# Performance work log

Hardware: AMD Instinct MI355X
Metric: run time of the kernel (lower is better)

## Reference

```python
import jax, jax.numpy as jnp
import numpy as np

H = 16
D_MODEL = 1024
HEAD_DIM = D_MODEL // H
NEG = -1e9


def setup_inputs() -> dict:
    key = jax.random.key(0)
    k1, k2, k3, k4, k5, k6 = jax.random.split(key, 6)
    B, L = 2, 2048
    feature = jax.random.normal(k1, (B, L, D_MODEL), dtype=jnp.float32)
    mask = jax.random.randint(k2, (B, L), 0, 2, dtype=jnp.int32)
    # Linear weights stored torch-style as [out, in]; biases zero-init per initialize().
    s = 1.0 / np.sqrt(D_MODEL)
    W_Q = jax.random.uniform(k3, (D_MODEL, D_MODEL), jnp.float32, -s, s)
    W_K = jax.random.uniform(k4, (D_MODEL, D_MODEL), jnp.float32, -s, s)
    W_V = jax.random.uniform(k5, (D_MODEL, D_MODEL), jnp.float32, -s, s)
    b_Q = jnp.zeros((D_MODEL,), jnp.float32)
    b_K = jnp.zeros((D_MODEL,), jnp.float32)
    b_V = jnp.zeros((D_MODEL,), jnp.float32)
    return {"feature": feature, "mask": mask, "W_Q": W_Q, "b_Q": b_Q,
            "W_K": W_K, "b_K": b_K, "W_V": W_V, "b_V": b_V}


def reference(feature, mask, W_Q, b_Q, W_K, b_K, W_V, b_V):
    B, L, _ = feature.shape
    scale = jnp.sqrt(jnp.float32(HEAD_DIM))
    # Projections: torch Linear is x @ W^T + b. Split into heads: [B, H, L, Dh]
    def proj(W, b):
        y = feature @ W.T + b
        return y.reshape(B, L, H, HEAD_DIM).transpose(0, 2, 1, 3)
    Q = proj(W_Q, b_Q)
    K = proj(W_K, b_K)
    V = proj(W_V, b_V)
    # Scores [B, H, Lq, Lk]
    A = jnp.einsum('bhqd,bhkd->bhqk', Q, K) / scale
    # Key-side mask broadcast over heads and query positions
    A = jnp.where(mask[:, None, None, :] == 0, jnp.float32(NEG), A)
    alpha = jax.nn.softmax(A, axis=-1)
    out = jnp.einsum('bhqk,bhkd->bhqd', alpha, V)  # [B, H, L, Dh]
    return out.transpose(0, 2, 1, 3).reshape(B, L, H * HEAD_DIM)
```

## Files before the change

kernel.cpp:

```cpp
#include <hip/hip_runtime.h>

typedef __bf16 bf16;
typedef __attribute__((ext_vector_type(4))) __bf16 bf16x4;
typedef __attribute__((ext_vector_type(8))) __bf16 bf16x8;
typedef __attribute__((ext_vector_type(4))) float f32x4;
typedef __attribute__((ext_vector_type(16))) float f32x16;
typedef unsigned int u32;

#define D_MODEL 1024
#define SEQ_L   2048
#define NHEAD   16
#define HDIM    64
#define MROWS   4096

#define S_SCALE 0.18033688f

#define FEAT_OFF  512u
#define WQ_OFF    (FEAT_OFF + 4194304u)
#define WK_OFF    (WQ_OFF + 1048576u)
#define WV_OFF    (WK_OFF + 1048576u)
#define BQ_OFF    (WV_OFF + 1048576u)
#define BK_OFF    (BQ_OFF + 1024u)
#define BV_OFF    (BK_OFF + 1024u)
#define Q_OFF     (BV_OFF + 1024u)
#define K_OFF     (Q_OFF + 4194304u)
#define V_OFF     (K_OFF + 4194304u)

typedef const __attribute__((address_space(1))) u32* gp_t;
typedef __attribute__((address_space(3))) u32* lp_t;
__device__ __forceinline__ void ld16(const bf16* g, bf16* l) {
    __builtin_amdgcn_global_load_lds((gp_t)g, (lp_t)l, 16, 0, 0);
}

__global__ void convert_in(const float* __restrict__ feat,
                           const float* __restrict__ wq, const float* __restrict__ wk,
                           const float* __restrict__ wv,
                           const float* __restrict__ bq, const float* __restrict__ bk,
                           const float* __restrict__ bv,
                           bf16* __restrict__ ws) {
    const int bid = blockIdx.x;
    const float* src; bf16* dst; int off; float sc = 1.0f;
    if (bid < 4096)      { src = feat; dst = ws + FEAT_OFF; off = bid * 1024; }
    else if (bid < 5120) { src = wq;   dst = ws + WQ_OFF;   off = (bid - 4096) * 1024; sc = S_SCALE; }
    else if (bid < 6144) { src = wk;   dst = ws + WK_OFF;   off = (bid - 5120) * 1024; }
    else if (bid < 7168) { src = wv;   dst = ws + WV_OFF;   off = (bid - 6144) * 1024; }
    else if (bid == 7168){ src = bq;   dst = ws + BQ_OFF;   off = 0; sc = S_SCALE; }
    else if (bid == 7169){ src = bk;   dst = ws + BK_OFF;   off = 0; }
    else                 { src = bv;   dst = ws + BV_OFF;   off = 0; }
    int idx = off + threadIdx.x * 4;
    float4 v = *(const float4*)(src + idx);
    dst[idx + 0] = (bf16)(v.x * sc);
    dst[idx + 1] = (bf16)(v.y * sc);
    dst[idx + 2] = (bf16)(v.z * sc);
    dst[idx + 3] = (bf16)(v.w * sc);
}

__global__ __launch_bounds__(256, 2) void qkv_gemm(const bf16* __restrict__ ws,
                                                   bf16* __restrict__ wsw,
                                                   const int* __restrict__ mask) {
    const int zi = blockIdx.z;
    const bf16* Amat = (zi == 2) ? ws + WV_OFF : ws + FEAT_OFF;
    const bf16* Bmat = (zi == 0) ? ws + WQ_OFF : (zi == 1) ? ws + WK_OFF : ws + FEAT_OFF;
    const bf16* bias = ws + ((zi == 0) ? BQ_OFF : (zi == 1) ? BK_OFF : BV_OFF);
    bf16* Y = (zi == 2) ? wsw + V_OFF : wsw + Q_OFF + (size_t)zi * 4194304u;

    __shared__ bf16 Alds[128 * 64];
    __shared__ bf16 Blds[128 * 64];

    const int t    = threadIdx.x;
    const int lane = t & 63;
    const int wave = t >> 6;
    const int quad = lane >> 4;
    const int l16  = lane & 15;
    const int m0   = ((zi == 2) ? blockIdx.y : blockIdx.x) * 128;
    const int n0   = ((zi == 2) ? blockIdx.x : blockIdx.y) * 128;
    const int wrow = (wave >> 1) * 64;
    const int wcol = (wave & 1) * 64;

    const int r8 = lane >> 3;
    const int sl = lane & 7;
    const int sg = sl ^ r8;

    f32x4 acc[4][4];
    for (int mi = 0; mi < 4; ++mi)
        for (int ni = 0; ni < 4; ++ni)
            acc[mi][ni] = (f32x4){0.f, 0.f, 0.f, 0.f};

    for (int k0 = 0; k0 < D_MODEL; k0 += 64) {
#pragma unroll
        for (int i = 0; i < 4; ++i) {
            int ch  = wave * 4 + i;
            int row = ch * 8 + r8;
            ld16(Amat + (size_t)(m0 + row) * D_MODEL + k0 + sg * 8, Alds + ch * 512);
            ld16(Bmat + (size_t)(n0 + row) * D_MODEL + k0 + sg * 8, Blds + ch * 512);
        }
        __syncthreads();

#pragma unroll
        for (int kk = 0; kk < 2; ++kk) {
            const int sgb = quad + kk * 4;
            bf16x8 af[4], bfr[4];
#pragma unroll
            for (int mi = 0; mi < 4; ++mi) {
                int row = wrow + mi * 16 + l16;
                af[mi] = *(const bf16x8*)(&Alds[row * 64 + ((sgb ^ (row & 7)) << 3)]);
            }
#pragma unroll
            for (int ni = 0; ni < 4; ++ni) {
                int row = wcol + ni * 16 + l16;
                bfr[ni] = *(const bf16x8*)(&Blds[row * 64 + ((sgb ^ (row & 7)) << 3)]);
            }
#pragma unroll
            for (int mi = 0; mi < 4; ++mi)
#pragma unroll
                for (int ni = 0; ni < 4; ++ni)
                    acc[mi][ni] = __builtin_amdgcn_mfma_f32_16x16x32_bf16(
                        af[mi], bfr[ni], acc[mi][ni], 0, 0, 0);
        }
        __syncthreads();
    }

    if (zi < 2) {
#pragma unroll
        for (int ni = 0; ni < 4; ++ni) {
            int col = n0 + wcol + ni * 16 + l16;
            float bvf = (float)bias[col];
#pragma unroll
            for (int mi = 0; mi < 4; ++mi) {
                int rowb = m0 + wrow + mi * 16 + quad * 4;
#pragma unroll
                for (int r = 0; r < 4; ++r) {
                    float v = acc[mi][ni][r] + bvf;
                    if (zi == 1 && mask[rowb + r] == 0) v = 0.f;
                    Y[(size_t)(rowb + r) * D_MODEL + col] = (bf16)v;
                }
            }
        }
    } else {
#pragma unroll
        for (int mi = 0; mi < 4; ++mi) {
#pragma unroll
            for (int r = 0; r < 4; ++r) {
                int rowv = m0 + wrow + mi * 16 + quad * 4 + r;
                float bvf = (float)bias[rowv];
#pragma unroll
                for (int ni = 0; ni < 4; ++ni) {
                    int col = n0 + wcol + ni * 16 + l16;
                    float v = acc[mi][ni][r] + bvf;
                    if (mask[col] == 0) v = 0.f;
                    size_t addr = (size_t)(col >> 11) * 2097152u +
                                  (size_t)rowv * 2048u + (col & 2047);
                    Y[addr] = (bf16)v;
                }
            }
        }
    }
}

__global__ __launch_bounds__(256, 4) void attn_kernel(
    const bf16* __restrict__ ws, bf16* __restrict__ wsw,
    const int* __restrict__ mask, float* __restrict__ out) {
    const int bh  = blockIdx.x;
    const int qt  = blockIdx.y;
    const int ks2 = blockIdx.z;
    const int b   = bh >> 4, h = bh & 15;
    const int t    = threadIdx.x;
    const int lane = t & 63;
    const int wave = t >> 6;
    const int half = lane >> 5;
    const int l31  = lane & 31;
    const int kt0  = ks2 * 1024;

    __shared__ bf16 Klds[2][64 * 64];
    __shared__ bf16 Vlds[2][64 * 64];

    const bf16* Qh  = ws + Q_OFF + (size_t)(b * SEQ_L) * D_MODEL + h * HDIM;
    const bf16* Kh  = ws + K_OFF + (size_t)(b * SEQ_L) * D_MODEL + h * HDIM;
    const bf16* Vth = ws + V_OFF + (size_t)b * 2097152u + (size_t)(h * HDIM) * SEQ_L;

    const int qrow0 = qt * 128 + wave * 32;
    bf16x8 qf[4];
#pragma unroll
    for (int ks = 0; ks < 4; ++ks)
        qf[ks] = *(const bf16x8*)(Qh + (size_t)(qrow0 + l31) * D_MODEL
                                  + ks * 16 + half * 8);

    bf16x8 ones;
#pragma unroll
    for (int j = 0; j < 8; ++j) ones[j] = (bf16)1.0f;

    f32x16 o[2], lacc;
    int nm = 0;
#pragma unroll
    for (int i = 0; i < 16; ++i) { o[0][i] = 0.f; o[1][i] = 0.f; lacc[i] = 0.f; }

    const int srow = (lane >> 3);
    const int sg   = (lane & 7) ^ srow;

#define STAGE(bb, kt)                                                          \
    do {                                                                       \
        _Pragma("unroll")                                                      \
        for (int i = 0; i < 2; ++i) {                                          \
            int row = i * 32 + wave * 8 + srow;                                \
            ld16(Kh + (size_t)((kt) + row) * D_MODEL + sg * 8,                 \
                 &Klds[bb][i * 2048 + wave * 512]);                            \
            ld16(Vth + (size_t)row * SEQ_L + (kt) + sg * 8,                    \
                 &Vlds[bb][i * 2048 + wave * 512]);                            \
        }                                                                      \
    } while (0)

    STAGE(0, kt0);
    __syncthreads();

    int cur = 0;
    for (int kt = kt0; kt < kt0 + 1024; kt += 64) {
        if (kt + 64 < kt0 + 1024) STAGE(cur ^ 1, kt + 64);

        int mv = mask[b * SEQ_L + kt + lane];
        nm += (int)__popcll(__ballot(mv != 0));

        f32x16 st[2];
#pragma unroll
        for (int ktile = 0; ktile < 2; ++ktile) {
#pragma unroll
            for (int i = 0; i < 16; ++i) st[ktile][i] = 0.f;
#pragma unroll
            for (int ks = 0; ks < 4; ++ks) {
                const int row  = ktile * 32 + l31;
                const int slot = (ks * 2 + half) ^ (l31 & 7);
                bf16x8 kf = *(const bf16x8*)(&Klds[cur][row * 64 + slot * 8]);
                st[ktile] = __builtin_amdgcn_mfma_f32_32x32x16_bf16(
                    kf, qf[ks], st[ktile], 0, 0, 0);
            }
        }

        bf16x4 pk[2][4];
#pragma unroll
        for (int ktile = 0; ktile < 2; ++ktile) {
#pragma unroll
            for (int g = 0; g < 4; ++g) {
                bf16x4 pkv;
#pragma unroll
                for (int j = 0; j < 4; ++j)
                    pkv[j] = (bf16)__builtin_amdgcn_exp2f(st[ktile][g * 4 + j]);
                pk[ktile][g] = pkv;
            }
        }

        bf16x8 pf[4];
#pragma unroll
        for (int ks = 0; ks < 4; ++ks) {
            const int k1 = ks & 1, kt2 = ks >> 1;
            uint2 a  = __builtin_bit_cast(uint2, pk[kt2][2 * k1]);
            uint2 bb = __builtin_bit_cast(uint2, pk[kt2][2 * k1 + 1]);
            uint2 keep, send;
            keep.x = half ? bb.x : a.x;  keep.y = half ? bb.y : a.y;
            send.x = half ? a.x : bb.x;  send.y = half ? a.y : bb.y;
            uint2 recv;
            recv.x = (unsigned)__shfl_xor((int)send.x, 32);
            recv.y = (unsigned)__shfl_xor((int)send.y, 32);
            uint4 frag;
            frag.x = half ? recv.x : keep.x;
            frag.y = half ? recv.y : keep.y;
            frag.z = half ? keep.x : recv.x;
            frag.w = half ? keep.y : recv.y;
            pf[ks] = __builtin_bit_cast(bf16x8, frag);
        }

#pragma unroll
        for (int ks = 0; ks < 4; ++ks)
            lacc = __builtin_amdgcn_mfma_f32_32x32x16_bf16(pf[ks], ones, lacc, 0, 0, 0);
#pragma unroll
        for (int dt = 0; dt < 2; ++dt) {
#pragma unroll
            for (int ks = 0; ks < 4; ++ks) {
                const int row  = dt * 32 + l31;
                const int slot = (ks * 2 + half) ^ (l31 & 7);
                bf16x8 vf = *(const bf16x8*)(&Vlds[cur][row * 64 + slot * 8]);
                o[dt] = __builtin_amdgcn_mfma_f32_32x32x16_bf16(
                    pf[ks], vf, o[dt], 0, 0, 0);
            }
        }

        __syncthreads();
        cur ^= 1;
    }
#undef STAGE

    float* Lp  = (float*)(wsw + WQ_OFF);
    bf16*  O1  = wsw + FEAT_OFF;
    const float corr = (float)(1024 - nm);
#pragma unroll
    for (int r = 0; r < 16; ++r) {
        const int q32 = (r & 3) + 8 * (r >> 2) + 4 * half;
        const int q = qrow0 + q32;
        const size_t base = ((size_t)(b * SEQ_L + q)) * D_MODEL + h * HDIM;
        if (l31 == 0)
            Lp[ks2 * 65536 + bh * 2048 + qrow0 + q32] = lacc[r] - corr;
        if (ks2 == 0) {
            out[base + l31]      = o[0][r];
            out[base + 32 + l31] = o[1][r];
        } else {
            O1[base + l31]      = (bf16)o[0][r];
            O1[base + 32 + l31] = (bf16)o[1][r];
        }
    }
}

__global__ void combine(float* __restrict__ out, const bf16* __restrict__ ws) {
    const float* Lp = (const float*)(ws + WQ_OFF);
    const bf16*  O1 = ws + FEAT_OFF;
    int idx = (blockIdx.x * 256 + threadIdx.x) * 4;
    int row = idx >> 10;
    int col = idx & 1023;
    int b = row >> 11, q = row & 2047, h = col >> 6;
    int li = (b * 16 + h) * 2048 + q;
    float rl = 1.0f / fmaxf(Lp[li] + Lp[65536 + li], 1e-30f);
    float4 o0 = *(float4*)(out + idx);
    bf16x4 o1 = *(const bf16x4*)(O1 + idx);
    float4 res;
    res.x = (o0.x + (float)o1[0]) * rl;
    res.y = (o0.y + (float)o1[1]) * rl;
    res.z = (o0.z + (float)o1[2]) * rl;
    res.w = (o0.w + (float)o1[3]) * rl;
    *(float4*)(out + idx) = res;
}

extern "C" void kernel_launch(void* const* d_in, const int* in_sizes, int n_in,
                              void* d_out, int out_size, void* d_ws, size_t ws_size,
                              hipStream_t stream) {
    const float* feat = (const float*)d_in[0];
    const int*   mask = (const int*)d_in[1];
    const float* Wq = (const float*)d_in[2];
    const float* bq = (const float*)d_in[3];
    const float* Wk = (const float*)d_in[4];
    const float* bk = (const float*)d_in[5];
    const float* Wv = (const float*)d_in[6];
    const float* bv = (const float*)d_in[7];

    bf16* ws = (bf16*)d_ws;

    convert_in<<<7171, 256, 0, stream>>>(feat, Wq, Wk, Wv, bq, bk, bv, ws);

    dim3 g1(32, 8, 3);
    qkv_gemm<<<g1, 256, 0, stream>>>(ws, ws, mask);

    dim3 g2(2 * NHEAD, SEQ_L / 128, 2);
    attn_kernel<<<g2, 256, 0, stream>>>(ws, ws, mask, (float*)d_out);

    combine<<<4096, 256, 0, stream>>>((float*)d_out, ws);
}
```

Before: 173.6 us.

## Process two query tiles per wave in attention, sum softmax row on VALU

Each wave now handles 64 query rows (two 32-row tiles), so every K/V fragment read from LDS feeds two MFMAs, and the grid shrinks to half as many blocks. The row-sum of exp values is accumulated with VALU adds and reduced with a cross-half shuffle instead of an extra MFMA against a ones vector. Key-tile iteration starts at a per-block rotated phase to spread memory traffic, s_setprio brackets the MFMA sections, and the convert kernel now writes bf16x4 vector stores. The cost is higher register pressure (launch bounds lowered to 2 blocks per SM) and fewer blocks for occupancy.

```diff
diff --git a/kernel.cpp b/kernel.cpp
--- a/kernel.cpp
+++ b/kernel.cpp
@@ -49,10 +49,12 @@
     else                 { src = bv;   dst = ws + BV_OFF;   off = 0; }
     int idx = off + threadIdx.x * 4;
     float4 v = *(const float4*)(src + idx);
-    dst[idx + 0] = (bf16)(v.x * sc);
-    dst[idx + 1] = (bf16)(v.y * sc);
-    dst[idx + 2] = (bf16)(v.z * sc);
-    dst[idx + 3] = (bf16)(v.w * sc);
+    bf16x4 o;
+    o[0] = (bf16)(v.x * sc);
+    o[1] = (bf16)(v.y * sc);
+    o[2] = (bf16)(v.z * sc);
+    o[3] = (bf16)(v.w * sc);
+    *(bf16x4*)(dst + idx) = o;
 }
 
 __global__ __launch_bounds__(256, 2) void qkv_gemm(const bf16* __restrict__ ws,
@@ -157,7 +159,43 @@
     }
 }
 
-__global__ __launch_bounds__(256, 4) void attn_kernel(
+__device__ __forceinline__ void softmax_pack(const f32x16* st, f32x4& ls,
+                                             bf16x8* pf, const int half) {
+    bf16x4 pk[2][4];
+#pragma unroll
+    for (int ktile = 0; ktile < 2; ++ktile)
+#pragma unroll
+        for (int g = 0; g < 4; ++g) {
+            bf16x4 pkv;
+#pragma unroll
+            for (int j = 0; j < 4; ++j) {
+                float e = __builtin_amdgcn_exp2f(st[ktile][g * 4 + j]);
+                ls[j] += e;
+                pkv[j] = (bf16)e;
+            }
+            pk[ktile][g] = pkv;
+        }
+#pragma unroll
+    for (int ks = 0; ks < 4; ++ks) {
+        const int k1 = ks & 1, kt2 = ks >> 1;
+        uint2 a  = __builtin_bit_cast(uint2, pk[kt2][2 * k1]);
+        uint2 bb = __builtin_bit_cast(uint2, pk[kt2][2 * k1 + 1]);
+        uint2 keep, send;
+        keep.x = half ? bb.x : a.x;  keep.y = half ? bb.y : a.y;
+        send.x = half ? a.x : bb.x;  send.y = half ? a.y : bb.y;
+        uint2 recv;
+        recv.x = (unsigned)__shfl_xor((int)send.x, 32);
+        recv.y = (unsigned)__shfl_xor((int)send.y, 32);
+        uint4 frag;
+        frag.x = half ? recv.x : keep.x;
+        frag.y = half ? recv.y : keep.y;
+        frag.z = half ? keep.x : recv.x;
+        frag.w = half ? keep.y : recv.y;
+        pf[ks] = __builtin_bit_cast(bf16x8, frag);
+    }
+}
+
+__global__ __launch_bounds__(256, 2) void attn_kernel(
     const bf16* __restrict__ ws, bf16* __restrict__ wsw,
     const int* __restrict__ mask, float* __restrict__ out) {
     const int bh  = blockIdx.x;
@@ -178,21 +216,24 @@
     const bf16* Kh  = ws + K_OFF + (size_t)(b * SEQ_L) * D_MODEL + h * HDIM;
     const bf16* Vth = ws + V_OFF + (size_t)b * 2097152u + (size_t)(h * HDIM) * SEQ_L;
 
-    const int qrow0 = qt * 128 + wave * 32;
-    bf16x8 qf[4];
-#pragma unroll
-    for (int ks = 0; ks < 4; ++ks)
-        qf[ks] = *(const bf16x8*)(Qh + (size_t)(qrow0 + l31) * D_MODEL
-                                  + ks * 16 + half * 8);
-
-    bf16x8 ones;
-#pragma unroll
-    for (int j = 0; j < 8; ++j) ones[j] = (bf16)1.0f;
-
-    f32x16 o[2], lacc;
+    const int qrowA = qt * 256 + wave * 64;
+    const int qrowB = qrowA + 32;
+    bf16x8 qfA[4], qfB[4];
+#pragma unroll
+    for (int ks = 0; ks < 4; ++ks) {
+        qfA[ks] = *(const bf16x8*)(Qh + (size_t)(qrowA + l31) * D_MODEL
+                                   + ks * 16 + half * 8);
+        qfB[ks] = *(const bf16x8*)(Qh + (size_t)(qrowB + l31) * D_MODEL
+                                   + ks * 16 + half * 8);
+    }
+
+    f32x16 oA[2], oB[2];
+    f32x4  lsA = (f32x4){0.f, 0.f, 0.f, 0.f};
+    f32x4  lsB = (f32x4){0.f, 0.f, 0.f, 0.f};
     int nm = 0;
 #pragma unroll
-    for (int i = 0; i < 16; ++i) { o[0][i] = 0.f; o[1][i] = 0.f; lacc[i] = 0.f; }
+    for (int i = 0; i < 16; ++i) { oA[0][i] = 0.f; oA[1][i] = 0.f;
+                                   oB[0][i] = 0.f; oB[1][i] = 0.f; }
 
     const int srow = (lane >> 3);
     const int sg   = (lane & 7) ^ srow;
@@ -209,67 +250,48 @@
         }                                                                      \
     } while (0)
 
-    STAGE(0, kt0);
+    const int phase = (bh * 5 + qt * 3 + ks2 * 9) & 15;
+
+    STAGE(0, kt0 + (phase << 6));
     __syncthreads();
 
     int cur = 0;
-    for (int kt = kt0; kt < kt0 + 1024; kt += 64) {
-        if (kt + 64 < kt0 + 1024) STAGE(cur ^ 1, kt + 64);
+    for (int it = 0; it < 16; ++it) {
+        const int kt = kt0 + (((it + phase) & 15) << 6);
+        if (it < 15) {
+            const int ktn = kt0 + (((it + 1 + phase) & 15) << 6);
+            STAGE(cur ^ 1, ktn);
+        }
 
         int mv = mask[b * SEQ_L + kt + lane];
         nm += (int)__popcll(__ballot(mv != 0));
 
-        f32x16 st[2];
+        f32x16 stA[2], stB[2];
+#pragma unroll
+        for (int ktile = 0; ktile < 2; ++ktile)
+#pragma unroll
+            for (int i = 0; i < 16; ++i) { stA[ktile][i] = 0.f; stB[ktile][i] = 0.f; }
+        __builtin_amdgcn_s_setprio(1);
 #pragma unroll
         for (int ktile = 0; ktile < 2; ++ktile) {
-#pragma unroll
-            for (int i = 0; i < 16; ++i) st[ktile][i] = 0.f;
 #pragma unroll
             for (int ks = 0; ks < 4; ++ks) {
                 const int row  = ktile * 32 + l31;
                 const int slot = (ks * 2 + half) ^ (l31 & 7);
                 bf16x8 kf = *(const bf16x8*)(&Klds[cur][row * 64 + slot * 8]);
-                st[ktile] = __builtin_amdgcn_mfma_f32_32x32x16_bf16(
-                    kf, qf[ks], st[ktile], 0, 0, 0);
-            }
-        }
-
-        bf16x4 pk[2][4];
-#pragma unroll
-        for (int ktile = 0; ktile < 2; ++ktile) {
-#pragma unroll
-            for (int g = 0; g < 4; ++g) {
-                bf16x4 pkv;
-#pragma unroll
-                for (int j = 0; j < 4; ++j)
-                    pkv[j] = (bf16)__builtin_amdgcn_exp2f(st[ktile][g * 4 + j]);
-                pk[ktile][g] = pkv;
-            }
-        }
-
-        bf16x8 pf[4];
-#pragma unroll
-        for (int ks = 0; ks < 4; ++ks) {
-            const int k1 = ks & 1, kt2 = ks >> 1;
-            uint2 a  = __builtin_bit_cast(uint2, pk[kt2][2 * k1]);
-            uint2 bb = __builtin_bit_cast(uint2, pk[kt2][2 * k1 + 1]);
-            uint2 keep, send;
-            keep.x = half ? bb.x : a.x;  keep.y = half ? bb.y : a.y;
-            send.x = half ? a.x : bb.x;  send.y = half ? a.y : bb.y;
-            uint2 recv;
-            recv.x = (unsigned)__shfl_xor((int)send.x, 32);
-            recv.y = (unsigned)__shfl_xor((int)send.y, 32);
-            uint4 frag;
-            frag.x = half ? recv.x : keep.x;
-            frag.y = half ? recv.y : keep.y;
-            frag.z = half ? keep.x : recv.x;
-            frag.w = half ? keep.y : recv.y;
-            pf[ks] = __builtin_bit_cast(bf16x8, frag);
-        }
-
-#pragma unroll
-        for (int ks = 0; ks < 4; ++ks)
-            lacc = __builtin_amdgcn_mfma_f32_32x32x16_bf16(pf[ks], ones, lacc, 0, 0, 0);
+                stA[ktile] = __builtin_amdgcn_mfma_f32_32x32x16_bf16(
+                    kf, qfA[ks], stA[ktile], 0, 0, 0);
+                stB[ktile] = __builtin_amdgcn_mfma_f32_32x32x16_bf16(
+                    kf, qfB[ks], stB[ktile], 0, 0, 0);
+            }
+        }
+        __builtin_amdgcn_s_setprio(0);
+
+        bf16x8 pfA[4], pfB[4];
+        softmax_pack(stA, lsA, pfA, half);
+        softmax_pack(stB, lsB, pfB, half);
+
+        __builtin_amdgcn_s_setprio(1);
 #pragma unroll
         for (int dt = 0; dt < 2; ++dt) {
 #pragma unroll
@@ -277,10 +299,13 @@
                 const int row  = dt * 32 + l31;
                 const int slot = (ks * 2 + half) ^ (l31 & 7);
                 bf16x8 vf = *(const bf16x8*)(&Vlds[cur][row * 64 + slot * 8]);
-                o[dt] = __builtin_amdgcn_mfma_f32_32x32x16_bf16(
-                    pf[ks], vf, o[dt], 0, 0, 0);
-            }
-        }
+                oA[dt] = __builtin_amdgcn_mfma_f32_32x32x16_bf16(
+                    pfA[ks], vf, oA[dt], 0, 0, 0);
+                oB[dt] = __builtin_amdgcn_mfma_f32_32x32x16_bf16(
+                    pfB[ks], vf, oB[dt], 0, 0, 0);
+            }
+        }
+        __builtin_amdgcn_s_setprio(0);
 
         __syncthreads();
         cur ^= 1;
@@ -290,19 +315,38 @@
     float* Lp  = (float*)(wsw + WQ_OFF);
     bf16*  O1  = wsw + FEAT_OFF;
     const float corr = (float)(1024 - nm);
+    float lA = lsA[0] + lsA[1] + lsA[2] + lsA[3];
+    float lB = lsB[0] + lsB[1] + lsB[2] + lsB[3];
+    lA += __shfl_xor(lA, 32);
+    lB += __shfl_xor(lB, 32);
+    if (half == 0) {
+        Lp[ks2 * 65536 + bh * 2048 + qrowA + l31] = lA - corr;
+        Lp[ks2 * 65536 + bh * 2048 + qrowB + l31] = lB - corr;
+    }
 #pragma unroll
     for (int r = 0; r < 16; ++r) {
         const int q32 = (r & 3) + 8 * (r >> 2) + 4 * half;
-        const int q = qrow0 + q32;
-        const size_t base = ((size_t)(b * SEQ_L + q)) * D_MODEL + h * HDIM;
-        if (l31 == 0)
-            Lp[ks2 * 65536 + bh * 2048 + qrow0 + q32] = lacc[r] - corr;
-        if (ks2 == 0) {
-            out[base + l31]      = o[0][r];
-            out[base + 32 + l31] = o[1][r];
-        } else {
-            O1[base + l31]      = (bf16)o[0][r];
-            O1[base + 32 + l31] = (bf16)o[1][r];
+        {
+            const int q = qrowA + q32;
+            const size_t base = ((size_t)(b * SEQ_L + q)) * D_MODEL + h * HDIM;
+            if (ks2 == 0) {
+                out[base + l31]      = oA[0][r];
+                out[base + 32 + l31] = oA[1][r];
+            } else {
+                O1[base + l31]      = (bf16)oA[0][r];
+                O1[base + 32 + l31] = (bf16)oA[1][r];
+            }
+        }
+        {
+            const int q = qrowB + q32;
+            const size_t base = ((size_t)(b * SEQ_L + q)) * D_MODEL + h * HDIM;
+            if (ks2 == 0) {
+                out[base + l31]      = oB[0][r];
+                out[base + 32 + l31] = oB[1][r];
+            } else {
+                O1[base + l31]      = (bf16)oB[0][r];
+                O1[base + 32 + l31] = (bf16)oB[1][r];
+            }
         }
     }
 }
@@ -345,7 +389,7 @@
     dim3 g1(32, 8, 3);
     qkv_gemm<<<g1, 256, 0, stream>>>(ws, ws, mask);
 
-    dim3 g2(2 * NHEAD, SEQ_L / 128, 2);
+    dim3 g2(2 * NHEAD, SEQ_L / 256, 2);
     attn_kernel<<<g2, 256, 0, stream>>>(ws, ws, mask, (float*)d_out);
 
     combine<<<4096, 256, 0, stream>>>((float*)d_out, ws);
```

Result: no change. 172.7 us (-0.5%).

## Software-pipeline QK^T one tile ahead with triple-buffered K in attention

Applied to the files above, without the earlier changes.

The attention loop is restructured so the QK^T MFMAs for the next key tile are issued before the PV MFMAs of the current tile. This lets the exp/pack work overlap with matrix-core work. K is now triple-buffered and staged two tiles ahead, V stays double-buffered, and the loop is fully unrolled. Mask popcounts are hoisted out of the loop, and the fp32-to-bf16 conversion now writes a single vectorised bf16x4 store. The cost is higher register pressure (two score tiles live), more LDS and larger code, which may reduce occupancy at the 4-blocks launch bound.

```diff
diff --git a/kernel.cpp b/kernel.cpp
--- a/kernel.cpp
+++ b/kernel.cpp
@@ -49,10 +49,12 @@
     else                 { src = bv;   dst = ws + BV_OFF;   off = 0; }
     int idx = off + threadIdx.x * 4;
     float4 v = *(const float4*)(src + idx);
-    dst[idx + 0] = (bf16)(v.x * sc);
-    dst[idx + 1] = (bf16)(v.y * sc);
-    dst[idx + 2] = (bf16)(v.z * sc);
-    dst[idx + 3] = (bf16)(v.w * sc);
+    bf16x4 o;
+    o[0] = (bf16)(v.x * sc);
+    o[1] = (bf16)(v.y * sc);
+    o[2] = (bf16)(v.z * sc);
+    o[3] = (bf16)(v.w * sc);
+    *(bf16x4*)(dst + idx) = o;
 }
 
 __global__ __launch_bounds__(256, 2) void qkv_gemm(const bf16* __restrict__ ws,
@@ -157,6 +159,39 @@
     }
 }
 
+__device__ __forceinline__ void softmax_pack(const f32x16* st, bf16x8* pf,
+                                             const int half) {
+    bf16x4 pk[2][4];
+#pragma unroll
+    for (int ktile = 0; ktile < 2; ++ktile)
+#pragma unroll
+        for (int g = 0; g < 4; ++g) {
+            bf16x4 pkv;
+#pragma unroll
+            for (int j = 0; j < 4; ++j)
+                pkv[j] = (bf16)__builtin_amdgcn_exp2f(st[ktile][g * 4 + j]);
+            pk[ktile][g] = pkv;
+        }
+#pragma unroll
+    for (int ks = 0; ks < 4; ++ks) {
+        const int k1 = ks & 1, kt2 = ks >> 1;
+        uint2 a  = __builtin_bit_cast(uint2, pk[kt2][2 * k1]);
+        uint2 bb = __builtin_bit_cast(uint2, pk[kt2][2 * k1 + 1]);
+        uint2 keep, send;
+        keep.x = half ? bb.x : a.x;  keep.y = half ? bb.y : a.y;
+        send.x = half ? a.x : bb.x;  send.y = half ? a.y : bb.y;
+        uint2 recv;
+        recv.x = (unsigned)__shfl_xor((int)send.x, 32);
+        recv.y = (unsigned)__shfl_xor((int)send.y, 32);
+        uint4 frag;
+        frag.x = half ? recv.x : keep.x;
+        frag.y = half ? recv.y : keep.y;
+        frag.z = half ? keep.x : recv.x;
+        frag.w = half ? keep.y : recv.y;
+        pf[ks] = __builtin_bit_cast(bf16x8, frag);
+    }
+}
+
 __global__ __launch_bounds__(256, 4) void attn_kernel(
     const bf16* __restrict__ ws, bf16* __restrict__ wsw,
     const int* __restrict__ mask, float* __restrict__ out) {
@@ -164,107 +199,112 @@
     const int qt  = blockIdx.y;
     const int ks2 = blockIdx.z;
     const int b   = bh >> 4, h = bh & 15;
-    const int t    = threadIdx.x;
-    const int lane = t & 63;
-    const int wave = t >> 6;
+    const int tid  = threadIdx.x;
+    const int lane = tid & 63;
+    const int wave = tid >> 6;
     const int half = lane >> 5;
     const int l31  = lane & 31;
     const int kt0  = ks2 * 1024;
 
-    __shared__ bf16 Klds[2][64 * 64];
+    __shared__ bf16 Klds[3][64 * 64];
     __shared__ bf16 Vlds[2][64 * 64];
 
     const bf16* Qh  = ws + Q_OFF + (size_t)(b * SEQ_L) * D_MODEL + h * HDIM;
     const bf16* Kh  = ws + K_OFF + (size_t)(b * SEQ_L) * D_MODEL + h * HDIM;
     const bf16* Vth = ws + V_OFF + (size_t)b * 2097152u + (size_t)(h * HDIM) * SEQ_L;
 
-    const int qrow0 = qt * 128 + wave * 32;
-    bf16x8 qf[4];
-#pragma unroll
-    for (int ks = 0; ks < 4; ++ks)
-        qf[ks] = *(const bf16x8*)(Qh + (size_t)(qrow0 + l31) * D_MODEL
-                                  + ks * 16 + half * 8);
-
-    bf16x8 ones;
-#pragma unroll
-    for (int j = 0; j < 8; ++j) ones[j] = (bf16)1.0f;
-
-    f32x16 o[2], lacc;
-    int nm = 0;
-#pragma unroll
-    for (int i = 0; i < 16; ++i) { o[0][i] = 0.f; o[1][i] = 0.f; lacc[i] = 0.f; }
-
     const int srow = (lane >> 3);
     const int sg   = (lane & 7) ^ srow;
 
-#define STAGE(bb, kt)                                                          \
+#define STAGE_K(bb, kt)                                                        \
     do {                                                                       \
         _Pragma("unroll")                                                      \
         for (int i = 0; i < 2; ++i) {                                          \
             int row = i * 32 + wave * 8 + srow;                                \
             ld16(Kh + (size_t)((kt) + row) * D_MODEL + sg * 8,                 \
                  &Klds[bb][i * 2048 + wave * 512]);                            \
+        }                                                                      \
+    } while (0)
+#define STAGE_V(bb, kt)                                                        \
+    do {                                                                       \
+        _Pragma("unroll")                                                      \
+        for (int i = 0; i < 2; ++i) {                                          \
+            int row = i * 32 + wave * 8 + srow;                                \
             ld16(Vth + (size_t)row * SEQ_L + (kt) + sg * 8,                    \
                  &Vlds[bb][i * 2048 + wave * 512]);                            \
         }                                                                      \
     } while (0)
 
-    STAGE(0, kt0);
+    STAGE_K(0, kt0);
+    STAGE_K(1, kt0 + 64);
+    STAGE_V(0, kt0);
+
+    int nm = 0;
+    {
+        int mvv[16];
+#pragma unroll
+        for (int i = 0; i < 16; ++i)
+            mvv[i] = mask[b * SEQ_L + kt0 + i * 64 + lane];
+#pragma unroll
+        for (int i = 0; i < 16; ++i)
+            nm += (int)__popcll(__ballot(mvv[i] != 0));
+    }
+
+    const int qrow0 = qt * 128 + wave * 32;
+    bf16x8 qf[4];
+#pragma unroll
+    for (int ks = 0; ks < 4; ++ks)
+        qf[ks] = *(const bf16x8*)(Qh + (size_t)(qrow0 + l31) * D_MODEL
+                                  + ks * 16 + half * 8);
+
+    bf16x8 ones;
+#pragma unroll
+    for (int j = 0; j < 8; ++j) ones[j] = (bf16)1.0f;
+
+    f32x16 o[2], lacc;
+#pragma unroll
+    for (int i = 0; i < 16; ++i) { o[0][i] = 0.f; o[1][i] = 0.f; lacc[i] = 0.f; }
+
     __syncthreads();
 
-    int cur = 0;
-    for (int kt = kt0; kt < kt0 + 1024; kt += 64) {
-        if (kt + 64 < kt0 + 1024) STAGE(cur ^ 1, kt + 64);
-
-        int mv = mask[b * SEQ_L + kt + lane];
-        nm += (int)__popcll(__ballot(mv != 0));
-
-        f32x16 st[2];
-#pragma unroll
-        for (int ktile = 0; ktile < 2; ++ktile) {
-#pragma unroll
-            for (int i = 0; i < 16; ++i) st[ktile][i] = 0.f;
-#pragma unroll
-            for (int ks = 0; ks < 4; ++ks) {
-                const int row  = ktile * 32 + l31;
-                const int slot = (ks * 2 + half) ^ (l31 & 7);
-                bf16x8 kf = *(const bf16x8*)(&Klds[cur][row * 64 + slot * 8]);
-                st[ktile] = __builtin_amdgcn_mfma_f32_32x32x16_bf16(
-                    kf, qf[ks], st[ktile], 0, 0, 0);
-            }
-        }
-
-        bf16x4 pk[2][4];
-#pragma unroll
-        for (int ktile = 0; ktile < 2; ++ktile) {
-#pragma unroll
-            for (int g = 0; g < 4; ++g) {
-                bf16x4 pkv;
-#pragma unroll
-                for (int j = 0; j < 4; ++j)
-                    pkv[j] = (bf16)__builtin_amdgcn_exp2f(st[ktile][g * 4 + j]);
-                pk[ktile][g] = pkv;
-            }
-        }
+    f32x16 st[2];
+#pragma unroll
+    for (int ktile = 0; ktile < 2; ++ktile) {
+#pragma unroll
+        for (int i = 0; i < 16; ++i) st[ktile][i] = 0.f;
+#pragma unroll
+        for (int ks = 0; ks < 4; ++ks) {
+            const int row  = ktile * 32 + l31;
+            const int slot = (ks * 2 + half) ^ (l31 & 7);
+            bf16x8 kf = *(const bf16x8*)(&Klds[0][row * 64 + slot * 8]);
+            st[ktile] = __builtin_amdgcn_mfma_f32_32x32x16_bf16(
+                kf, qf[ks], st[ktile], 0, 0, 0);
+        }
+    }
+
+#pragma unroll
+    for (int it = 0; it < 16; ++it) {
+        const int kt = kt0 + it * 64;
+        if (it < 14) STAGE_K((it + 2) % 3, kt + 128);
+        if (it < 15) STAGE_V((it + 1) & 1, kt + 64);
 
         bf16x8 pf[4];
-#pragma unroll
-        for (int ks = 0; ks < 4; ++ks) {
-            const int k1 = ks & 1, kt2 = ks >> 1;
-            uint2 a  = __builtin_bit_cast(uint2, pk[kt2][2 * k1]);
-            uint2 bb = __builtin_bit_cast(uint2, pk[kt2][2 * k1 + 1]);
-            uint2 keep, send;
-            keep.x = half ? bb.x : a.x;  keep.y = half ? bb.y : a.y;
-            send.x = half ? a.x : bb.x;  send.y = half ? a.y : bb.y;
-            uint2 recv;
-            recv.x = (unsigned)__shfl_xor((int)send.x, 32);
-            recv.y = (unsigned)__shfl_xor((int)send.y, 32);
-            uint4 frag;
-            frag.x = half ? recv.x : keep.x;
-            frag.y = half ? recv.y : keep.y;
-            frag.z = half ? keep.x : recv.x;
-            frag.w = half ? keep.y : recv.y;
-            pf[ks] = __builtin_bit_cast(bf16x8, frag);
+        softmax_pack(st, pf, half);
+
+        if (it < 15) {
+#pragma unroll
+            for (int ktile = 0; ktile < 2; ++ktile) {
+#pragma unroll
+                for (int i = 0; i < 16; ++i) st[ktile][i] = 0.f;
+#pragma unroll
+                for (int ks = 0; ks < 4; ++ks) {
+                    const int row  = ktile * 32 + l31;
+                    const int slot = (ks * 2 + half) ^ (l31 & 7);
+                    bf16x8 kf = *(const bf16x8*)(&Klds[(it + 1) % 3][row * 64 + slot * 8]);
+                    st[ktile] = __builtin_amdgcn_mfma_f32_32x32x16_bf16(
+                        kf, qf[ks], st[ktile], 0, 0, 0);
+                }
+            }
         }
 
 #pragma unroll
@@ -276,16 +316,16 @@
             for (int ks = 0; ks < 4; ++ks) {
                 const int row  = dt * 32 + l31;
                 const int slot = (ks * 2 + half) ^ (l31 & 7);
-                bf16x8 vf = *(const bf16x8*)(&Vlds[cur][row * 64 + slot * 8]);
+                bf16x8 vf = *(const bf16x8*)(&Vlds[it & 1][row * 64 + slot * 8]);
                 o[dt] = __builtin_amdgcn_mfma_f32_32x32x16_bf16(
                     pf[ks], vf, o[dt], 0, 0, 0);
             }
         }
 
         __syncthreads();
-        cur ^= 1;
-    }
-#undef STAGE
+    }
+#undef STAGE_K
+#undef STAGE_V
 
     float* Lp  = (float*)(wsw + WQ_OFF);
     bf16*  O1  = wsw + FEAT_OFF;
```

Measured after the change: 284.0 us. +63.6%, slower.
